# Kernel optimization log

Hardware: AMD Instinct MI355X
Metric: run time of the kernel (lower is better)

The kernel has to match this reference:

```python
import jax, jax.numpy as jnp
import numpy as np

N_HEAD = 16
HEAD = 64
EMBED = 1024
TOP_K_RATIO = 0.1
MASKED = True
B, T = 2, 2048


def setup_inputs() -> dict:
    key = jax.random.key(0)
    ks = jax.random.split(key, 7)
    w = lambda k, shape: jax.random.normal(k, shape, jnp.float32) * 0.02
    return {
        "index": jax.random.normal(ks[0], (B, T, EMBED), jnp.float32),
        "memory": jax.random.normal(ks[1], (B, T, EMBED), jnp.float32),
        "Wq": w(ks[2], (N_HEAD, EMBED, HEAD)),
        "Wk": w(ks[3], (N_HEAD, EMBED, HEAD)),
        "Wv": w(ks[4], (N_HEAD, EMBED, HEAD)),
        "W_proj": w(ks[5], (N_HEAD * HEAD, EMBED)),
        "b_proj": jnp.zeros((EMBED,), jnp.float32),
    }


def reference(index, memory, Wq, Wk, Wv, W_proj, b_proj):
    b, t, e = index.shape
    s = memory.shape[1]
    # All heads batched: [B, H, T, D]
    q = jnp.einsum("bte,hed->bhtd", index, Wq)
    k = jnp.einsum("bse,hed->bhsd", memory, Wk)
    v = jnp.einsum("bse,hed->bhsd", memory, Wv)
    scores = jnp.einsum("bhtd,bhsd->bhts", q, k) * (HEAD ** -0.5)  # [B,H,T,S]
    neg_inf = jnp.array(-jnp.inf, scores.dtype)
    if MASKED:
        causal = jnp.tril(jnp.ones((t, s), bool))
        scores = jnp.where(causal, scores, neg_inf)
    # top-k sparsification: keep only the top ceil(ratio*S) scores per query row
    k_top = max(1, int(TOP_K_RATIO * s))
    thresh = jax.lax.top_k(scores, k_top)[0][..., -1:]  # kth largest per row
    scores = jnp.where(scores >= thresh, scores, neg_inf)
    att = jax.nn.softmax(scores, axis=-1)
    out = jnp.einsum("bhts,bhsd->bhtd", att, v)
    # concat heads along feature dim: [B, T, H*D]
    out = out.transpose(0, 2, 1, 3).reshape(b, t, N_HEAD * HEAD)
    return out @ W_proj + b_proj  # dropout is identity at eval
```

## Files before the change

### kernel.cpp

```cpp
#include <hip/hip_runtime.h>
#include <hip/hip_bf16.h>

#define TT 2048
#define KTOP 204
#define ROWS 16
#define SCS 2056
#define HSTR 130

typedef float f32x4 __attribute__((ext_vector_type(4)));
typedef short short8 __attribute__((ext_vector_type(8)));
typedef unsigned short u16;
typedef unsigned int u32;
typedef u32 u32x2 __attribute__((ext_vector_type(2)));
typedef u32 u32x4 __attribute__((ext_vector_type(4)));

static __device__ __forceinline__ f32x4 mfma16(short8 a, short8 b, f32x4 c) {
  return __builtin_amdgcn_mfma_f32_16x16x32_bf16(a, b, c, 0, 0, 0);
}

static __device__ __forceinline__ u16 f2b(float f) {
  __hip_bfloat16 h = __float2bfloat16(f);
  return *reinterpret_cast<u16*>(&h);
}

static __device__ __forceinline__ u32 cvt_pk_bf16(float lo, float hi) {
  u32 r;
  asm("v_cvt_pk_bf16_f32 %0, %1, %2" : "=v"(r) : "v"(lo), "v"(hi));
  return r;
}

#define GLOAD16(gp, lp) __builtin_amdgcn_global_load_lds( \
    (const __attribute__((address_space(1))) void*)(gp),  \
    (__attribute__((address_space(3))) void*)(lp), 16, 0, 0)

#define WSYNC() do { __builtin_amdgcn_wave_barrier(); \
    asm volatile("s_waitcnt lgkmcnt(0)" ::: "memory"); \
    __builtin_amdgcn_wave_barrier(); } while (0)

static __device__ __forceinline__ void radix_rank(int h0, int h1c, int h2c,
                                                  int h3c, int lane, int& k,
                                                  u32& digOut) {
  int lsum = h0 + h1c + h2c + h3c;
  int ssum = lsum;
#pragma unroll
  for (int off = 1; off < 64; off <<= 1) {
    int o = __shfl_down(ssum, off);
    ssum += (lane + off < 64) ? o : 0;
  }
  int above = ssum - lsum;
  int cg3 = above;
  int cg2 = cg3 + h3c;
  int cg1 = cg2 + h2c;
  int cg0 = cg1 + h1c;
  int idx = lane * 4;
  int dig = -1, nk = 0;
  if (cg0 < k && cg0 + h0 >= k) { dig = idx;     nk = k - cg0; }
  if (cg1 < k && cg1 + h1c >= k) { dig = idx + 1; nk = k - cg1; }
  if (cg2 < k && cg2 + h2c >= k) { dig = idx + 2; nk = k - cg2; }
  if (cg3 < k && cg3 + h3c >= k) { dig = idx + 3; nk = k - cg3; }
  unsigned long long ball = __ballot(dig >= 0);
  int src = __ffsll((long long)ball) - 1;
  dig = __shfl(dig, src);
  nk = __shfl(nk, src);
  digOut = (u32)dig;
  k = nk;
}

template <int JMAX>
static __device__ __forceinline__ void select_softmax(
    u16* __restrict__ sc, const u32* __restrict__ hist8,
    u32* __restrict__ h2w, float* __restrict__ rs, int w, int lane, int t0) {
  const int NI = JMAX * 4;
  int row0 = w, row1 = w + 8;
  bool sel0 = t0 + row0 + 1 > KTOP, sel1 = t0 + row1 + 1 > KTOP;

  u32 rv0[NI], rv1[NI];
#pragma unroll
  for (int j = 0; j < JMAX; ++j) {
    u32x4 v0 = *(const u32x4*)&sc[row0 * SCS + lane * 8 + j * 512];
    u32x4 v1 = *(const u32x4*)&sc[row1 * SCS + lane * 8 + j * 512];
    rv0[j*4+0] = v0[0]; rv0[j*4+1] = v0[1]; rv0[j*4+2] = v0[2]; rv0[j*4+3] = v0[3];
    rv1[j*4+0] = v1[0]; rv1[j*4+1] = v1[1]; rv1[j*4+2] = v1[2]; rv1[j*4+3] = v1[3];
  }

  u32 a0w = hist8[row0 * HSTR + lane * 2], a1w = hist8[row0 * HSTR + lane * 2 + 1];
  u32 b0w = hist8[row1 * HSTR + lane * 2], b1w = hist8[row1 * HSTR + lane * 2 + 1];

  int lt0 = lane * 4 + ((a1w >> 16) ? 3 : ((a1w & 0xFFFFu) ? 2
                       : ((a0w >> 16) ? 1 : 0)));
  int lt1 = lane * 4 + ((b1w >> 16) ? 3 : ((b1w & 0xFFFFu) ? 2
                       : ((b0w >> 16) ? 1 : 0)));
  unsigned long long bl0 = __ballot((a0w | a1w) != 0);
  unsigned long long bl1 = __ballot((b0w | b1w) != 0);
  int top0 = __shfl(lt0, 63 - __builtin_clzll(bl0));
  int top1 = __shfl(lt1, 63 - __builtin_clzll(bl1));
  u32 ref0 = ((u32)top0 << 8) + 255u;
  u32 ref1 = ((u32)top1 << 8) + 255u;

  u32 keyth0 = 0, keyth1 = 0;
  int k0 = KTOP, k1 = KTOP;
  u32 d1_0 = 0, d1_1 = 0, d;
  if (sel0) {
    radix_rank((int)(a0w & 0xFFFF), (int)(a0w >> 16),
               (int)(a1w & 0xFFFF), (int)(a1w >> 16), lane, k0, d1_0);
  }
  if (sel1) {
    radix_rank((int)(b0w & 0xFFFF), (int)(b0w >> 16),
               (int)(b1w & 0xFFFF), (int)(b1w >> 16), lane, k1, d1_1);
  }

  if (sel0) {
    h2w[lane] = 0; h2w[lane + 64] = 0;
    WSYNC();
#pragma unroll
    for (int i = 0; i < NI; ++i) {
      u32 p = rv0[i];
      u32 e0 = p & 0xFFFFu, e1 = p >> 16;
      if ((e0 >> 8) == d1_0)
        atomicAdd(&h2w[(e0 & 255u) >> 1], 1u << ((e0 & 1u) << 4));
      if ((e1 >> 8) == d1_0)
        atomicAdd(&h2w[(e1 & 255u) >> 1], 1u << ((e1 & 1u) << 4));
    }
    WSYNC();
    u32 w0 = h2w[lane * 2], w1 = h2w[lane * 2 + 1];
    radix_rank((int)(w0 & 0xFFFF), (int)(w0 >> 16),
               (int)(w1 & 0xFFFF), (int)(w1 >> 16), lane, k0, d);
    keyth0 = (d1_0 << 8) | d;
  }
  if (sel1) {
    h2w[lane] = 0; h2w[lane + 64] = 0;
    WSYNC();
#pragma unroll
    for (int i = 0; i < NI; ++i) {
      u32 p = rv1[i];
      u32 e0 = p & 0xFFFFu, e1 = p >> 16;
      if ((e0 >> 8) == d1_1)
        atomicAdd(&h2w[(e0 & 255u) >> 1], 1u << ((e0 & 1u) << 4));
      if ((e1 >> 8) == d1_1)
        atomicAdd(&h2w[(e1 & 255u) >> 1], 1u << ((e1 & 1u) << 4));
    }
    WSYNC();
    u32 w0 = h2w[lane * 2], w1 = h2w[lane * 2 + 1];
    radix_rank((int)(w0 & 0xFFFF), (int)(w0 >> 16),
               (int)(w1 & 0xFFFF), (int)(w1 >> 16), lane, k1, d);
    keyth1 = (d1_1 << 8) | d;
  }

  u32 thr0 = keyth0 > 1u ? keyth0 : 1u;
  u32 thr1 = keyth1 > 1u ? keyth1 : 1u;
  const float c2 = 1.44269504f / 4096.f;
  float sum0 = 0.f, sum1 = 0.f;
#pragma unroll
  for (int i = 0; i < NI; ++i) {
    u32 p0 = rv0[i], p1 = rv1[i];
    u32 a0 = p0 & 0xFFFFu, a1 = p0 >> 16;
    u32 b0 = p1 & 0xFFFFu, b1 = p1 >> 16;
    float pa0 = (a0 >= thr0) ? exp2f((float)(int)(a0 - ref0) * c2) : 0.f;
    float pa1 = (a1 >= thr0) ? exp2f((float)(int)(a1 - ref0) * c2) : 0.f;
    float pb0 = (b0 >= thr1) ? exp2f((float)(int)(b0 - ref1) * c2) : 0.f;
    float pb1 = (b1 >= thr1) ? exp2f((float)(int)(b1 - ref1) * c2) : 0.f;
    sum0 += pa0 + pa1;
    sum1 += pb0 + pb1;
    rv0[i] = cvt_pk_bf16(pa0, pa1);
    rv1[i] = cvt_pk_bf16(pb0, pb1);
  }
#pragma unroll
  for (int off = 32; off; off >>= 1) {
    sum0 += __shfl_xor(sum0, off);
    sum1 += __shfl_xor(sum1, off);
  }
#pragma unroll
  for (int j = 0; j < JMAX; ++j) {
    *(u32x4*)&sc[row0 * SCS + lane * 8 + j * 512] =
        (u32x4){rv0[j*4+0], rv0[j*4+1], rv0[j*4+2], rv0[j*4+3]};
    *(u32x4*)&sc[row1 * SCS + lane * 8 + j * 512] =
        (u32x4){rv1[j*4+0], rv1[j*4+1], rv1[j*4+2], rv1[j*4+3]};
  }
  if (lane == 0) {
    rs[row0] = 1.f / fmaxf(sum0, 1e-30f);
    rs[row1] = 1.f / fmaxf(sum1, 1e-30f);
  }
}


__global__ __launch_bounds__(256) void k_cast2(const float* __restrict__ in0,
                                               const float* __restrict__ in1,
                                               u16* __restrict__ o0,
                                               u16* __restrict__ o1) {
  const float* in = blockIdx.z ? in1 : in0;
  u16* out = blockIdx.z ? o1 : o0;
  int i = (blockIdx.x * 256 + threadIdx.x) * 4;
  f32x4 v = *(const f32x4*)(in + i);
  u16 r0 = f2b(v[0]), r1 = f2b(v[1]), r2 = f2b(v[2]), r3 = f2b(v[3]);
  out[i] = r0; out[i+1] = r1; out[i+2] = r2; out[i+3] = r3;
}

__global__ __launch_bounds__(256) void k_tw3(
    const float* __restrict__ W0, const float* __restrict__ W1,
    const float* __restrict__ W2, u16* __restrict__ o0,
    u16* __restrict__ o1, u16* __restrict__ o2) {
  int z = blockIdx.z;
  const float* W = z == 0 ? W0 : (z == 1 ? W1 : W2);
  u16* out = z == 0 ? o0 : (z == 1 ? o1 : o2);
  int i = blockIdx.x * 256 + threadIdx.x;
  int d = i & 63, e = (i >> 6) & 1023, h = i >> 16;
  out[(h * 64 + d) * 1024 + e] = f2b(W[i]);
}

__global__ __launch_bounds__(256) void k_tsq(const float* __restrict__ W,
                                             u16* __restrict__ out) {
  int i = blockIdx.x * 256 + threadIdx.x;
  int n = i & 1023, kk = i >> 10;
  out[n * 1024 + kk] = f2b(W[i]);
}

static __device__ __forceinline__ void gemm_core(
    const u16* __restrict__ A, const u16* __restrict__ Bt, int m0, int n0,
    int tid, u16 (*lA)[2048], u16 (*lB)[2048], f32x4* acc) {
  const int K = 1024;
  int w = tid >> 6, lane = tid & 63;
  int lr = lane & 15, lg = lane >> 4;
  const u16* ga = A + (size_t)(m0 + (tid >> 2)) * K + (tid & 3) * 8;
  const u16* gb = Bt + (size_t)(n0 + (tid >> 2)) * K + (tid & 3) * 8;
  char* a0 = (char*)lA[0] + w * 1024;
  char* a1 = (char*)lA[1] + w * 1024;
  char* b0 = (char*)lB[0] + w * 1024;
  char* b1 = (char*)lB[1] + w * 1024;

  for (int kt = 0; kt < K; kt += 64) {
    __syncthreads();
    GLOAD16(ga + kt, a0);
    GLOAD16(gb + kt, b0);
    GLOAD16(ga + kt + 32, a1);
    GLOAD16(gb + kt + 32, b1);
    __syncthreads();
#pragma unroll
    for (int p = 0; p < 2; ++p) {
      short8 a = *(const short8*)&lA[p][(w * 16 + lr) * 32 + lg * 8];
#pragma unroll
      for (int j = 0; j < 4; ++j) {
        short8 b = *(const short8*)&lB[p][(j * 16 + lr) * 32 + lg * 8];
        acc[j] = mfma16(a, b, acc[j]);
      }
    }
  }
}

__global__ __launch_bounds__(256) void gemm_qkv(
    const u16* __restrict__ xbi, const u16* __restrict__ xbm,
    const u16* __restrict__ wqt, const u16* __restrict__ wkt,
    const u16* __restrict__ wvt, u16* __restrict__ qb,
    u16* __restrict__ kbf, u16* __restrict__ vtb) {
  __shared__ u16 lA[2][2048], lB[2][2048];
  int tid = threadIdx.x, z = blockIdx.z;
  int m0 = blockIdx.y * 64, n0 = blockIdx.x * 64;
  const u16* A = z ? xbm : xbi;
  const u16* Bt = z == 0 ? wqt : (z == 1 ? wkt : wvt);
  f32x4 acc[4] = {};
  gemm_core(A, Bt, m0, n0, tid, lA, lB, acc);

  int w = tid >> 6, lane = tid & 63, lr = lane & 15, lg = lane >> 4;
  float ascale = (z == 0) ? 0.125f : 1.f;
  u16* out0 = (z == 0) ? qb : kbf;
  int mbase = m0 + w * 16 + lg * 4;
#pragma unroll
  for (int j = 0; j < 4; ++j) {
    int n = n0 + j * 16 + lr;
#pragma unroll
    for (int jj = 0; jj < 4; ++jj) {
      int m = mbase + jj;
      float v = acc[j][jj];
      int b = m >> 11, t = m & 2047, h = n >> 6, dd = n & 63;
      if (z == 2)
        vtb[(((size_t)(b * 16 + h)) * 64 + dd) * TT + t] = f2b(v);
      else
        out0[(((size_t)(b * 16 + h)) * TT + t) * 64 + dd] = f2b(v * ascale);
    }
  }
}

__global__ __launch_bounds__(256) void gemm_proj(
    const u16* __restrict__ A, const u16* __restrict__ Bt,
    float* __restrict__ outp, const float* __restrict__ bias) {
  __shared__ u16 lA[2][2048], lB[2][2048];
  int tid = threadIdx.x;
  int m0 = blockIdx.y * 64, n0 = blockIdx.x * 64;
  f32x4 acc[4] = {};
  gemm_core(A, Bt, m0, n0, tid, lA, lB, acc);

  int w = tid >> 6, lane = tid & 63, lr = lane & 15, lg = lane >> 4;
  int mbase = m0 + w * 16 + lg * 4;
#pragma unroll
  for (int j = 0; j < 4; ++j) {
    int n = n0 + j * 16 + lr;
#pragma unroll
    for (int jj = 0; jj < 4; ++jj) {
      int m = mbase + jj;
      outp[(size_t)m * 1024 + n] = acc[j][jj] + bias[n];
    }
  }
}

__global__ __launch_bounds__(512, 4) void k_attn(
    const u16* __restrict__ qb, const u16* __restrict__ kb,
    const u16* __restrict__ vtb, u16* __restrict__ aob) {
  __shared__ u16 sc[ROWS * SCS];
  __shared__ u32 aux[3104];
  __shared__ float rs[ROWS];

  u32* hist8 = aux;
  u32* h2 = aux + 2080;

  int tid = threadIdx.x, w = tid >> 6, lane = tid & 63;
  int lr = lane & 15, lg = lane >> 4;
  int bid = blockIdx.x + 128 * blockIdx.y;
  int swz = (bid & 7) * 512 + (bid >> 3);
  int t0 = (swz & 127) * ROWS;
  int bh = swz >> 7;
  const u16* qh = qb + (size_t)bh * TT * 64;
  const u16* kh = kb + (size_t)bh * TT * 64;
  const u16* vh = vtb + (size_t)bh * 64 * TT;
  int SC = ((t0 + ROWS + 31) >> 5) << 5;
  int jmax = (SC + 511) >> 9;

  for (int i = tid; i < ROWS * HSTR; i += 512) hist8[i] = 0;

  short8 qf0 = *(const short8*)&qh[(size_t)(t0 + lr) * 64 + lg * 8];
  short8 qf1 = *(const short8*)&qh[(size_t)(t0 + lr) * 64 + 32 + lg * 8];
  __syncthreads();

  {
    int t = t0 + lr;
    int s0 = w * 16;
    short8 kc0, kc1, kn0, kn1;
    if (s0 < SC) {
      kc0 = *(const short8*)&kh[(size_t)(s0 + lr) * 64 + lg * 8];
      kc1 = *(const short8*)&kh[(size_t)(s0 + lr) * 64 + 32 + lg * 8];
      if (s0 + 128 < SC) {
        kn0 = *(const short8*)&kh[(size_t)(s0 + 128 + lr) * 64 + lg * 8];
        kn1 = *(const short8*)&kh[(size_t)(s0 + 128 + lr) * 64 + 32 + lg * 8];
      }
    }
    for (; s0 < SC; s0 += 128) {
      f32x4 acc = {0.f, 0.f, 0.f, 0.f};
      acc = mfma16(kc0, qf0, acc);
      acc = mfma16(kc1, qf1, acc);
      kc0 = kn0; kc1 = kn1;
      if (s0 + 256 < SC) {
        kn0 = *(const short8*)&kh[(size_t)(s0 + 256 + lr) * 64 + lg * 8];
        kn1 = *(const short8*)&kh[(size_t)(s0 + 256 + lr) * 64 + 32 + lg * 8];
      }
      int sbase = s0 + lg * 4;
      u32 key[4];
      if (s0 + 15 <= t0) {
#pragma unroll
        for (int j = 0; j < 4; ++j) {
          float kf = fmaf(acc[j], 4096.f, 32768.f);
          key[j] = (u32)fminf(fmaxf(kf, 0.f), 65535.f);
        }
      } else {
#pragma unroll
        for (int j = 0; j < 4; ++j) {
          float kf = fmaf(acc[j], 4096.f, 32768.f);
          key[j] = (u32)fminf(fmaxf(kf, 0.f), 65535.f);
          if (sbase + j > t) key[j] = 0;
        }
      }
#pragma unroll
      for (int j = 0; j < 4; ++j)
        atomicAdd(&hist8[lr * HSTR + (key[j] >> 9)],
                  1u << (((key[j] >> 8) & 1u) << 4));
      *(u32x2*)&sc[lr * SCS + sbase] =
          (u32x2){key[0] | (key[1] << 16), key[2] | (key[3] << 16)};
    }
  }
  {
    int fillEnd = jmax << 9;
    for (int r = 0; r < ROWS; ++r)
      for (int s = SC + tid * 8; s < fillEnd; s += 512 * 8)
        *(u32x4*)&sc[r * SCS + s] = (u32x4){0, 0, 0, 0};
  }
  __syncthreads();

  switch (jmax) {
    case 1: select_softmax<1>(sc, hist8, &h2[w * 128], rs, w, lane, t0); break;
    case 2: select_softmax<2>(sc, hist8, &h2[w * 128], rs, w, lane, t0); break;
    case 3: select_softmax<3>(sc, hist8, &h2[w * 128], rs, w, lane, t0); break;
    default: select_softmax<4>(sc, hist8, &h2[w * 128], rs, w, lane, t0); break;
  }
  __syncthreads();

  float* po = (float*)aux;
  int d0 = (w & 3) * 16;
  int h = w >> 2;
  int tiles = SC >> 5;
  int mid = ((tiles + 1) >> 1) << 5;
  int kb0 = h ? mid : 0;
  int kb1 = h ? SC : mid;
  f32x4 o = {0.f, 0.f, 0.f, 0.f};
  {
    int kk = kb0;
    short8 bn;
    if (kk < kb1)
      bn = *(const short8*)&vh[(size_t)(d0 + lr) * TT + kk + lg * 8];
    for (; kk < kb1; kk += 32) {
      short8 b = bn;
      int kn = kk + 32;
      if (kn < kb1)
        bn = *(const short8*)&vh[(size_t)(d0 + lr) * TT + kn + lg * 8];
      short8 a = *(const short8*)&sc[lr * SCS + kk + lg * 8];
      o = mfma16(a, b, o);
    }
  }
#pragma unroll
  for (int j = 0; j < 4; ++j)
    po[(h * ROWS + lg * 4 + j) * 68 + d0 + lr] = o[j];
  __syncthreads();

  if (w < 4) {
    int b_ = bh >> 4, h_ = bh & 15;
    int dd0 = w * 16;
#pragma unroll
    for (int j = 0; j < 4; ++j) {
      int row = lg * 4 + j;
      float val = (po[row * 68 + dd0 + lr] + po[(ROWS + row) * 68 + dd0 + lr]) *
                  rs[row];
      aob[((size_t)(b_ * TT + t0 + row)) * 1024 + h_ * 64 + dd0 + lr] = f2b(val);
    }
  }
}


extern "C" void kernel_launch(void* const* d_in, const int* in_sizes, int n_in,
                              void* d_out, int out_size, void* d_ws, size_t ws_size,
                              hipStream_t stream) {
  const float* index  = (const float*)d_in[0];
  const float* memory = (const float*)d_in[1];
  const float* Wq     = (const float*)d_in[2];
  const float* Wk     = (const float*)d_in[3];
  const float* Wv     = (const float*)d_in[4];
  const float* Wp     = (const float*)d_in[5];
  const float* bp     = (const float*)d_in[6];

  char* ws = (char*)d_ws;
  const size_t MB = 1024 * 1024;
  u16* xbi = (u16*)(ws + 0);
  u16* xbm = (u16*)(ws + 8 * MB);
  u16* wqt = (u16*)(ws + 16 * MB);
  u16* wkt = (u16*)(ws + 18 * MB);
  u16* wvt = (u16*)(ws + 20 * MB);
  u16* wpt = (u16*)(ws + 22 * MB);
  u16* qb  = (u16*)(ws + 24 * MB);
  u16* kbf = (u16*)(ws + 32 * MB);
  u16* vtb = (u16*)(ws + 40 * MB);
  u16* aob = xbi;

  k_cast2<<<dim3(4096, 1, 2), 256, 0, stream>>>(index, memory, xbi, xbm);
  k_tw3<<<dim3(4096, 1, 3), 256, 0, stream>>>(Wq, Wk, Wv, wqt, wkt, wvt);
  k_tsq<<<4096, 256, 0, stream>>>(Wp, wpt);

  gemm_qkv<<<dim3(16, 64, 3), 256, 0, stream>>>(xbi, xbm, wqt, wkt, wvt,
                                                qb, kbf, vtb);

  k_attn<<<dim3(128, 32), 512, 0, stream>>>(qb, kbf, vtb, aob);

  gemm_proj<<<dim3(16, 64), 256, 0, stream>>>(aob, wpt, (float*)d_out, bp);
}
```

Baseline: 281.8 us.

## Merge prep kernels, reverse block order, skip masked QK tiles, unroll PV

```diff
diff --git a/kernel.cpp b/kernel.cpp
--- a/kernel.cpp
+++ b/kernel.cpp
@@ -182,36 +182,30 @@
   }
 }
 
-
-__global__ __launch_bounds__(256) void k_cast2(const float* __restrict__ in0,
-                                               const float* __restrict__ in1,
-                                               u16* __restrict__ o0,
-                                               u16* __restrict__ o1) {
-  const float* in = blockIdx.z ? in1 : in0;
-  u16* out = blockIdx.z ? o1 : o0;
-  int i = (blockIdx.x * 256 + threadIdx.x) * 4;
-  f32x4 v = *(const f32x4*)(in + i);
-  u16 r0 = f2b(v[0]), r1 = f2b(v[1]), r2 = f2b(v[2]), r3 = f2b(v[3]);
-  out[i] = r0; out[i+1] = r1; out[i+2] = r2; out[i+3] = r3;
-}
-
-__global__ __launch_bounds__(256) void k_tw3(
-    const float* __restrict__ W0, const float* __restrict__ W1,
-    const float* __restrict__ W2, u16* __restrict__ o0,
-    u16* __restrict__ o1, u16* __restrict__ o2) {
+__global__ __launch_bounds__(256) void k_prep(
+    const float* __restrict__ index, const float* __restrict__ memory,
+    const float* __restrict__ Wq, const float* __restrict__ Wk,
+    const float* __restrict__ Wv, const float* __restrict__ Wp,
+    u16* __restrict__ xbi, u16* __restrict__ xbm, u16* __restrict__ wqt,
+    u16* __restrict__ wkt, u16* __restrict__ wvt, u16* __restrict__ wpt) {
   int z = blockIdx.z;
-  const float* W = z == 0 ? W0 : (z == 1 ? W1 : W2);
-  u16* out = z == 0 ? o0 : (z == 1 ? o1 : o2);
   int i = blockIdx.x * 256 + threadIdx.x;
-  int d = i & 63, e = (i >> 6) & 1023, h = i >> 16;
-  out[(h * 64 + d) * 1024 + e] = f2b(W[i]);
-}
-
-__global__ __launch_bounds__(256) void k_tsq(const float* __restrict__ W,
-                                             u16* __restrict__ out) {
-  int i = blockIdx.x * 256 + threadIdx.x;
-  int n = i & 1023, kk = i >> 10;
-  out[n * 1024 + kk] = f2b(W[i]);
+  if (z < 2) {
+    const float* in = z ? memory : index;
+    u16* out = z ? xbm : xbi;
+    int i4 = i * 4;
+    f32x4 v = *(const f32x4*)(in + i4);
+    u16 r0 = f2b(v[0]), r1 = f2b(v[1]), r2 = f2b(v[2]), r3 = f2b(v[3]);
+    out[i4] = r0; out[i4+1] = r1; out[i4+2] = r2; out[i4+3] = r3;
+  } else if (z < 5) {
+    const float* W = z == 2 ? Wq : (z == 3 ? Wk : Wv);
+    u16* out = z == 2 ? wqt : (z == 3 ? wkt : wvt);
+    int d = i & 63, e = (i >> 6) & 1023, h = i >> 16;
+    out[(h * 64 + d) * 1024 + e] = f2b(W[i]);
+  } else {
+    int n = i & 1023, kk = i >> 10;
+    wpt[n * 1024 + kk] = f2b(Wp[i]);
+  }
 }
 
 static __device__ __forceinline__ void gemm_core(
@@ -314,7 +308,7 @@
   int tid = threadIdx.x, w = tid >> 6, lane = tid & 63;
   int lr = lane & 15, lg = lane >> 4;
   int bid = blockIdx.x + 128 * blockIdx.y;
-  int swz = (bid & 7) * 512 + (bid >> 3);
+  int swz = (bid & 7) * 512 + (511 - (bid >> 3));
   int t0 = (swz & 127) * ROWS;
   int bh = swz >> 7;
   const u16* qh = qb + (size_t)bh * TT * 64;
@@ -331,47 +325,100 @@
 
   {
     int t = t0 + lr;
-    int s0 = w * 16;
-    short8 kc0, kc1, kn0, kn1;
+    int tmax = t0 + 15;
+    u32* hrow = &hist8[lr * HSTR];
+    u16* srow = &sc[lr * SCS];
+    int s0 = w * 32;
+    short8 cA0, cA1, cB0, cB1, nA0, nA1, nB0, nB1;
     if (s0 < SC) {
-      kc0 = *(const short8*)&kh[(size_t)(s0 + lr) * 64 + lg * 8];
-      kc1 = *(const short8*)&kh[(size_t)(s0 + lr) * 64 + 32 + lg * 8];
-      if (s0 + 128 < SC) {
-        kn0 = *(const short8*)&kh[(size_t)(s0 + 128 + lr) * 64 + lg * 8];
-        kn1 = *(const short8*)&kh[(size_t)(s0 + 128 + lr) * 64 + 32 + lg * 8];
-      }
-    }
-    for (; s0 < SC; s0 += 128) {
-      f32x4 acc = {0.f, 0.f, 0.f, 0.f};
-      acc = mfma16(kc0, qf0, acc);
-      acc = mfma16(kc1, qf1, acc);
-      kc0 = kn0; kc1 = kn1;
-      if (s0 + 256 < SC) {
-        kn0 = *(const short8*)&kh[(size_t)(s0 + 256 + lr) * 64 + lg * 8];
-        kn1 = *(const short8*)&kh[(size_t)(s0 + 256 + lr) * 64 + 32 + lg * 8];
-      }
-      int sbase = s0 + lg * 4;
-      u32 key[4];
-      if (s0 + 15 <= t0) {
-#pragma unroll
-        for (int j = 0; j < 4; ++j) {
-          float kf = fmaf(acc[j], 4096.f, 32768.f);
-          key[j] = (u32)fminf(fmaxf(kf, 0.f), 65535.f);
+      if (s0 <= tmax) {
+        cA0 = *(const short8*)&kh[(size_t)(s0 + lr) * 64 + lg * 8];
+        cA1 = *(const short8*)&kh[(size_t)(s0 + lr) * 64 + 32 + lg * 8];
+      }
+      if (s0 + 16 <= tmax) {
+        cB0 = *(const short8*)&kh[(size_t)(s0 + 16 + lr) * 64 + lg * 8];
+        cB1 = *(const short8*)&kh[(size_t)(s0 + 16 + lr) * 64 + 32 + lg * 8];
+      }
+    }
+    for (; s0 < SC; s0 += 256) {
+      int sn = s0 + 256;
+      if (sn < SC) {
+        if (sn <= tmax) {
+          nA0 = *(const short8*)&kh[(size_t)(sn + lr) * 64 + lg * 8];
+          nA1 = *(const short8*)&kh[(size_t)(sn + lr) * 64 + 32 + lg * 8];
         }
-      } else {
-#pragma unroll
-        for (int j = 0; j < 4; ++j) {
-          float kf = fmaf(acc[j], 4096.f, 32768.f);
-          key[j] = (u32)fminf(fmaxf(kf, 0.f), 65535.f);
-          if (sbase + j > t) key[j] = 0;
+        if (sn + 16 <= tmax) {
+          nB0 = *(const short8*)&kh[(size_t)(sn + 16 + lr) * 64 + lg * 8];
+          nB1 = *(const short8*)&kh[(size_t)(sn + 16 + lr) * 64 + 32 + lg * 8];
         }
       }
-#pragma unroll
-      for (int j = 0; j < 4; ++j)
-        atomicAdd(&hist8[lr * HSTR + (key[j] >> 9)],
-                  1u << (((key[j] >> 8) & 1u) << 4));
-      *(u32x2*)&sc[lr * SCS + sbase] =
-          (u32x2){key[0] | (key[1] << 16), key[2] | (key[3] << 16)};
+      bool cmpA = s0 <= tmax;
+      bool cmpB = s0 + 16 <= tmax;
+      f32x4 accA = {0.f, 0.f, 0.f, 0.f};
+      f32x4 accB = {0.f, 0.f, 0.f, 0.f};
+      if (cmpA) {
+        accA = mfma16(cA0, qf0, accA);
+        accA = mfma16(cA1, qf1, accA);
+      }
+      if (cmpB) {
+        accB = mfma16(cB0, qf0, accB);
+        accB = mfma16(cB1, qf1, accB);
+      }
+      {
+        int sbase = s0 + lg * 4;
+        if (cmpA) {
+          u32 key[4];
+          if (s0 + 15 <= t0) {
+#pragma unroll
+            for (int j = 0; j < 4; ++j) {
+              float kf = fmaf(accA[j], 4096.f, 32768.f);
+              key[j] = (u32)fminf(fmaxf(kf, 0.f), 65535.f);
+            }
+          } else {
+#pragma unroll
+            for (int j = 0; j < 4; ++j) {
+              float kf = fmaf(accA[j], 4096.f, 32768.f);
+              key[j] = (u32)fminf(fmaxf(kf, 0.f), 65535.f);
+              if (sbase + j > t) key[j] = 0;
+            }
+          }
+#pragma unroll
+          for (int j = 0; j < 4; ++j)
+            atomicAdd(&hrow[key[j] >> 9], 1u << (((key[j] >> 8) & 1u) << 4));
+          *(u32x2*)&srow[sbase] =
+              (u32x2){key[0] | (key[1] << 16), key[2] | (key[3] << 16)};
+        } else {
+          *(u32x2*)&srow[sbase] = (u32x2){0u, 0u};
+        }
+      }
+      {
+        int sbase = s0 + 16 + lg * 4;
+        if (cmpB) {
+          u32 key[4];
+          if (s0 + 31 <= t0) {
+#pragma unroll
+            for (int j = 0; j < 4; ++j) {
+              float kf = fmaf(accB[j], 4096.f, 32768.f);
+              key[j] = (u32)fminf(fmaxf(kf, 0.f), 65535.f);
+            }
+          } else {
+#pragma unroll
+            for (int j = 0; j < 4; ++j) {
+              float kf = fmaf(accB[j], 4096.f, 32768.f);
+              key[j] = (u32)fminf(fmaxf(kf, 0.f), 65535.f);
+              if (sbase + j > t) key[j] = 0;
+            }
+          }
+#pragma unroll
+          for (int j = 0; j < 4; ++j)
+            atomicAdd(&hrow[key[j] >> 9], 1u << (((key[j] >> 8) & 1u) << 4));
+          *(u32x2*)&srow[sbase] =
+              (u32x2){key[0] | (key[1] << 16), key[2] | (key[3] << 16)};
+        } else {
+          *(u32x2*)&srow[sbase] = (u32x2){0u, 0u};
+        }
+      }
+      cA0 = nA0; cA1 = nA1; cB0 = nB0; cB1 = nB1;
     }
   }
   {
@@ -397,21 +444,27 @@
   int mid = ((tiles + 1) >> 1) << 5;
   int kb0 = h ? mid : 0;
   int kb1 = h ? SC : mid;
-  f32x4 o = {0.f, 0.f, 0.f, 0.f};
+  f32x4 o0 = {0.f, 0.f, 0.f, 0.f};
+  f32x4 o1 = {0.f, 0.f, 0.f, 0.f};
   {
+    const u16* vrow = &vh[(size_t)(d0 + lr) * TT];
+    const u16* prow = &sc[lr * SCS];
     int kk = kb0;
-    short8 bn;
-    if (kk < kb1)
-      bn = *(const short8*)&vh[(size_t)(d0 + lr) * TT + kk + lg * 8];
-    for (; kk < kb1; kk += 32) {
-      short8 b = bn;
-      int kn = kk + 32;
-      if (kn < kb1)
-        bn = *(const short8*)&vh[(size_t)(d0 + lr) * TT + kn + lg * 8];
-      short8 a = *(const short8*)&sc[lr * SCS + kk + lg * 8];
-      o = mfma16(a, b, o);
-    }
-  }
+    for (; kk + 32 < kb1; kk += 64) {
+      short8 b0 = *(const short8*)&vrow[kk + lg * 8];
+      short8 b1 = *(const short8*)&vrow[kk + 32 + lg * 8];
+      short8 a0 = *(const short8*)&prow[kk + lg * 8];
+      short8 a1 = *(const short8*)&prow[kk + 32 + lg * 8];
+      o0 = mfma16(a0, b0, o0);
+      o1 = mfma16(a1, b1, o1);
+    }
+    if (kk < kb1) {
+      short8 b0 = *(const short8*)&vrow[kk + lg * 8];
+      short8 a0 = *(const short8*)&prow[kk + lg * 8];
+      o0 = mfma16(a0, b0, o0);
+    }
+  }
+  f32x4 o = o0 + o1;
 #pragma unroll
   for (int j = 0; j < 4; ++j)
     po[(h * ROWS + lg * 4 + j) * 68 + d0 + lr] = o[j];
@@ -455,9 +508,8 @@
   u16* vtb = (u16*)(ws + 40 * MB);
   u16* aob = xbi;
 
-  k_cast2<<<dim3(4096, 1, 2), 256, 0, stream>>>(index, memory, xbi, xbm);
-  k_tw3<<<dim3(4096, 1, 3), 256, 0, stream>>>(Wq, Wk, Wv, wqt, wkt, wvt);
-  k_tsq<<<4096, 256, 0, stream>>>(Wp, wpt);
+  k_prep<<<dim3(4096, 1, 6), 256, 0, stream>>>(index, memory, Wq, Wk, Wv, Wp,
+                                               xbi, xbm, wqt, wkt, wvt, wpt);
 
   gemm_qkv<<<dim3(16, 64, 3), 256, 0, stream>>>(xbi, xbm, wqt, wkt, wvt,
                                                 qb, kbf, vtb);
```

Result: no change. 285.2 us (+1.2%).
